# Performance work log

Hardware: AMD Instinct MI355X
Metric: run time of the kernel (lower is better)

Reference implementation:

```python
import jax, jax.numpy as jnp
import numpy as np

DIM = 1  # module init arg; scale = 1/dim**(-0.5) = sqrt(dim)


def setup_inputs() -> dict:
    key = jax.random.key(0)
    kq, kk, kv, km = jax.random.split(key, 4)
    B, Sq, Sk, D = 8, 2048, 2048, 128
    q = jax.random.normal(kq, (B, Sq, D), dtype=jnp.float32)
    k = jax.random.normal(kk, (B, Sk, D), dtype=jnp.float32)
    v = jax.random.normal(kv, (B, Sk, D), dtype=jnp.float32)
    mask = jax.random.uniform(km, (B, Sq, Sk), dtype=jnp.float32)
    return {"q": q, "k": k, "v": v, "mask": mask}


def reference(q, k, v, mask):
    # q = q / dim**(-0.5)  ==  q * sqrt(dim)
    q = q * (DIM ** 0.5)
    # [B, Sq, Sk] scores, multiplicative mask BEFORE softmax
    scores = jnp.einsum("bqd,bkd->bqk", q, k) * mask
    attn = jax.nn.softmax(scores, axis=-1)
    return jnp.einsum("bqk,bkd->bqd", attn, v)
```

## Files before the change

kernel.cpp:

```cpp
#include <hip/hip_runtime.h>
#include <math.h>


typedef short bf16x8 __attribute__((ext_vector_type(8)));
typedef short short4v __attribute__((ext_vector_type(4)));
typedef float f32x4 __attribute__((ext_vector_type(4)));
typedef unsigned short u16x4 __attribute__((ext_vector_type(4)));

#define MFMA16 __builtin_amdgcn_mfma_f32_16x16x32_bf16

namespace {
constexpr int SKn = 2048, DH = 128;
constexpr int QB = 64;
constexpr int NSTEP = 32;

__device__ __forceinline__ unsigned short f2bf(float f) {
    union { float f; unsigned u; } x; x.f = f;
    unsigned r = x.u + 0x7FFFu + ((x.u >> 16) & 1u);
    return (unsigned short)(r >> 16);
}
__device__ __forceinline__ float bf2f(unsigned short h) {
    union { unsigned u; float f; } x; x.u = ((unsigned)h) << 16;
    return x.f;
}
}

__global__ __launch_bounds__(512, 2) void fattn_kernel(
    const float* __restrict__ Q, const float* __restrict__ K,
    const float* __restrict__ V, const float* __restrict__ M,
    float* __restrict__ O)
{
    __shared__ __align__(16) char smem[131072];
    const int bid = blockIdx.x;
    const int b  = bid & 7;
    const int qt = bid >> 3;
    const int tid = threadIdx.x;
    const int lane = tid & 63;
    const int w = tid >> 6;
    const int g2 = w >> 2;
    const int wq = w & 3;
    const int gtid = tid & 255;
    const int m16 = lane & 15;
    const int g = lane >> 4;

    char* slotbase = smem + g2 * 65536;

    const float* Qw = Q + ((size_t)(b * 2048 + qt * QB + wq * 16)) * DH;
    const float* Kb = K + (size_t)b * SKn * DH;
    const float* Vb = V + (size_t)b * SKn * DH;
    const float* Mw = M + ((size_t)(b * 2048 + qt * QB + wq * 16)) * SKn;
    float* Ow = O + ((size_t)(b * 2048 + qt * QB + wq * 16)) * DH;

    bf16x8 qh[4], ql[4];
#pragma unroll
    for (int c = 0; c < 4; ++c) {
        const float* qp = Qw + m16 * DH + c * 32 + g * 8;
        f32x4 a0 = *(const f32x4*)qp;
        f32x4 a1 = *(const f32x4*)(qp + 4);
#pragma unroll
        for (int j = 0; j < 8; ++j) {
            float x = (j < 4) ? a0[j] : a1[j - 4];
            unsigned short h = f2bf(x);
            qh[c][j] = (short)h;
            ql[c][j] = (short)f2bf(x - bf2f(h));
        }
    }

    f32x4 kreg[4], vreg[4];
    f32x4 mreg[2], mreg2[2];
    const int krow = gtid >> 5, kc4 = gtid & 31;
    const int vkv = gtid & 31,  vc8 = gtid >> 5;

    auto kv_of = [&](int t) { return (2 * t + g2) * 32; };

    auto stage_load = [&](int t) {
        const int kv0 = kv_of(t);
#pragma unroll
        for (int i = 0; i < 4; ++i)
            kreg[i] = *(const f32x4*)(Kb + (size_t)(kv0 + i * 8 + krow) * DH + kc4 * 4);
#pragma unroll
        for (int i = 0; i < 4; ++i)
            vreg[i] = *(const f32x4*)(Vb + (size_t)(kv0 + vkv) * DH + (vc8 + i * 8) * 4);
    };

    auto stage_write = [&](int bufsel) {
        char* Khi = slotbase + bufsel * 32768;
        char* Klo = Khi + 8192;
        char* Vhi = Khi + 16384;
        char* Vlo = Khi + 24576;
#pragma unroll
        for (int i = 0; i < 4; ++i) {
            const int row = i * 8 + krow;
            u16x4 h4, l4;
#pragma unroll
            for (int j = 0; j < 4; ++j) {
                unsigned short h = f2bf(kreg[i][j]);
                h4[j] = h;
                l4[j] = f2bf(kreg[i][j] - bf2f(h));
            }
            const int off = row * 256 + ((kc4 * 8) ^ ((row & 15) << 4));
            *(u16x4*)(Khi + off) = h4;
            *(u16x4*)(Klo + off) = l4;
        }
#pragma unroll
        for (int i = 0; i < 4; ++i) {
#pragma unroll
            for (int j = 0; j < 4; ++j) {
                const int d = (vc8 + i * 8) * 4 + j;
                const int off = d * 64 + ((vkv * 2) ^ ((d & 7) << 3));
                unsigned short h = f2bf(vreg[i][j]);
                *(unsigned short*)(Vhi + off) = h;
                *(unsigned short*)(Vlo + off) = f2bf(vreg[i][j] - bf2f(h));
            }
        }
    };

    auto mload = [&](int t, f32x4* dst) {
        const int kv0 = kv_of(t);
#pragma unroll
        for (int nt = 0; nt < 2; ++nt)
            dst[nt] = *(const f32x4*)(Mw + (size_t)m16 * SKn + kv0 + nt * 16 + 4 * g);
    };

    f32x4 o_[8];
#pragma unroll
    for (int nt = 0; nt < 8; ++nt) o_[nt] = 0.f;
    float mrow = -INFINITY, lrow = 0.f;

    stage_load(0);
    mload(0, mreg);
    stage_write(0);
    __syncthreads();

    for (int t = 0; t < NSTEP; ++t) {
        const int cur = t & 1;
        const bool more = (t + 1 < NSTEP);
        if (more) stage_load(t + 1);

        const char* Khi = slotbase + cur * 32768;
        const char* Klo = Khi + 8192;
        f32x4 sT[2];
        sT[0] = 0.f; sT[1] = 0.f;
#pragma unroll
        for (int c = 0; c < 4; ++c) {
#pragma unroll
            for (int nt = 0; nt < 2; ++nt) {
                const int row = nt * 16 + m16;
                const int off = row * 256 + ((c * 64 + g * 16) ^ ((row & 15) << 4));
                bf16x8 ah = *(const bf16x8*)(Khi + off);
                bf16x8 al = *(const bf16x8*)(Klo + off);
                sT[nt] = MFMA16(ah, qh[c], sT[nt], 0, 0, 0);
                sT[nt] = MFMA16(ah, ql[c], sT[nt], 0, 0, 0);
                sT[nt] = MFMA16(al, qh[c], sT[nt], 0, 0, 0);
            }
        }

        if (more) mload(t + 1, mreg2);

        float p[2][4];
        float mx = -INFINITY;
#pragma unroll
        for (int nt = 0; nt < 2; ++nt)
#pragma unroll
            for (int r = 0; r < 4; ++r) {
                p[nt][r] = sT[nt][r] * mreg[nt][r];
                mx = fmaxf(mx, p[nt][r]);
            }
        mx = fmaxf(mx, __shfl_xor(mx, 16));
        mx = fmaxf(mx, __shfl_xor(mx, 32));
        const float mn = fmaxf(mrow, mx);
        const float corr = __expf(mrow - mn);
        mrow = mn;
        float ps = 0.f;
#pragma unroll
        for (int nt = 0; nt < 2; ++nt)
#pragma unroll
            for (int r = 0; r < 4; ++r) {
                p[nt][r] = __expf(p[nt][r] - mn);
                ps += p[nt][r];
            }
        ps += __shfl_xor(ps, 16);
        ps += __shfl_xor(ps, 32);
        lrow = lrow * corr + ps;

        f32x4 corrO;
#pragma unroll
        for (int r = 0; r < 4; ++r) corrO[r] = __shfl(corr, 4 * g + r);
#pragma unroll
        for (int nt = 0; nt < 8; ++nt)
#pragma unroll
            for (int r = 0; r < 4; ++r) o_[nt][r] *= corrO[r];

        bf16x8 ph, pl;
#pragma unroll
        for (int e = 0; e < 8; ++e) {
            const float x = p[e >> 2][e & 3];
            unsigned short h = f2bf(x);
            ph[e] = (short)h;
            pl[e] = (short)f2bf(x - bf2f(h));
        }

        const char* Vhi = Khi + 16384;
        const char* Vlo = Khi + 24576;
#pragma unroll
        for (int nt = 0; nt < 8; ++nt) {
            const int d = nt * 16 + m16;
            const int sw = (d & 7) << 3;
            const int off1 = d * 64 + ((g * 8) ^ sw);
            const int off2 = d * 64 + ((32 + g * 8) ^ sw);
            short4v h1 = *(const short4v*)(Vhi + off1);
            short4v h2 = *(const short4v*)(Vhi + off2);
            short4v l1 = *(const short4v*)(Vlo + off1);
            short4v l2 = *(const short4v*)(Vlo + off2);
            bf16x8 vh = __builtin_shufflevector(h1, h2, 0, 1, 2, 3, 4, 5, 6, 7);
            bf16x8 vl = __builtin_shufflevector(l1, l2, 0, 1, 2, 3, 4, 5, 6, 7);
            o_[nt] = MFMA16(ph, vh, o_[nt], 0, 0, 0);
            o_[nt] = MFMA16(ph, vl, o_[nt], 0, 0, 0);
            o_[nt] = MFMA16(pl, vh, o_[nt], 0, 0, 0);
        }

        if (more) stage_write(cur ^ 1);
        __syncthreads();
        if (more) { mreg[0] = mreg2[0]; mreg[1] = mreg2[1]; }
    }

    if (g2 == 1) {
        char* ob = smem + wq * 8448;
#pragma unroll
        for (int nt = 0; nt < 8; ++nt)
#pragma unroll
            for (int r = 0; r < 4; ++r)
                *(float*)(ob + (4 * g + r) * 528 + (nt * 16 + m16) * 4) = o_[nt][r];
        if (g == 0)
            *(float2*)(smem + 33792 + wq * 128 + m16 * 8) = make_float2(mrow, lrow);
    }
    __syncthreads();
    if (g2 == 0) {
        const float2 ml1 = *(const float2*)(smem + 33792 + wq * 128 + m16 * 8);
        const float ms = fmaxf(mrow, ml1.x);
        const float e0 = __expf(mrow - ms);
        const float e1 = __expf(ml1.x - ms);
        const float inv = 1.f / (lrow * e0 + ml1.y * e1);
        const float a0 = e0 * inv, a1 = e1 * inv;
        f32x4 a0r, a1r;
#pragma unroll
        for (int r = 0; r < 4; ++r) {
            a0r[r] = __shfl(a0, 4 * g + r);
            a1r[r] = __shfl(a1, 4 * g + r);
        }
        const char* ob = smem + wq * 8448;
#pragma unroll
        for (int nt = 0; nt < 8; ++nt)
#pragma unroll
            for (int r = 0; r < 4; ++r) {
                const int d = nt * 16 + m16;
                const float o1 = *(const float*)(ob + (4 * g + r) * 528 + d * 4);
                Ow[(size_t)(4 * g + r) * DH + d] = o_[nt][r] * a0r[r] + o1 * a1r[r];
            }
    }
}

extern "C" void kernel_launch(void* const* d_in, const int* in_sizes, int n_in,
                              void* d_out, int out_size, void* d_ws, size_t ws_size,
                              hipStream_t stream) {
    (void)in_sizes; (void)n_in; (void)out_size; (void)d_ws; (void)ws_size;
    const float* q = (const float*)d_in[0];
    const float* k = (const float*)d_in[1];
    const float* v = (const float*)d_in[2];
    const float* m = (const float*)d_in[3];
    float* o = (float*)d_out;
    fattn_kernel<<<dim3(256), dim3(512), 0, stream>>>(q, k, v, m, o);
}
```

Baseline: 274.3 us.

## Split KV range across two blocks with merge kernel, single-buffer LDS

Splits the key/value sequence into two halves processed by separate blocks, doubling the grid to 512 blocks, and writes partial outputs plus max/sum stats to workspace. A new merge kernel combines the two halves. LDS is halved to a single buffer (double buffering removed, two barriers per step) so more blocks fit per CU, and the bf16 hi/lo split now uses truncation via perm instead of round-to-nearest. The mask is prefetched two steps ahead and MFMA sections get raised priority. The cost is extra workspace traffic, a second launch, and less load/compute overlap.

```diff
diff --git a/kernel.cpp b/kernel.cpp
--- a/kernel.cpp
+++ b/kernel.cpp
@@ -5,14 +5,16 @@
 typedef short bf16x8 __attribute__((ext_vector_type(8)));
 typedef short short4v __attribute__((ext_vector_type(4)));
 typedef float f32x4 __attribute__((ext_vector_type(4)));
-typedef unsigned short u16x4 __attribute__((ext_vector_type(4)));
 
 #define MFMA16 __builtin_amdgcn_mfma_f32_16x16x32_bf16
 
 namespace {
 constexpr int SKn = 2048, DH = 128;
 constexpr int QB = 64;
-constexpr int NSTEP = 32;
+constexpr int ROWS = 8 * 2048;
+constexpr size_t OPART_BYTES = 2ull * ROWS * DH * 4;
+constexpr size_t ML_BYTES = 2ull * ROWS * 8;
+constexpr size_t WS_NEED = OPART_BYTES + ML_BYTES;
 
 __device__ __forceinline__ unsigned short f2bf(float f) {
     union { float f; unsigned u; } x; x.f = f;
@@ -25,15 +27,18 @@
 }
 }
 
-__global__ __launch_bounds__(512, 2) void fattn_kernel(
+__global__ __launch_bounds__(512, 4) void fattn_kernel(
     const float* __restrict__ Q, const float* __restrict__ K,
     const float* __restrict__ V, const float* __restrict__ M,
-    float* __restrict__ O)
+    float* __restrict__ Oout, float2* __restrict__ MLout, const int nkvh)
 {
-    __shared__ __align__(16) char smem[131072];
+    __shared__ __align__(16) char smem[65536];
     const int bid = blockIdx.x;
     const int b  = bid & 7;
-    const int qt = bid >> 3;
+    const int rest = bid >> 3;
+    const int kvh = rest % nkvh;
+    const int qt = rest / nkvh;
+    const int nstep = 16 * (2 / nkvh) * 2 / 2;
     const int tid = threadIdx.x;
     const int lane = tid & 63;
     const int w = tid >> 6;
@@ -43,13 +48,14 @@
     const int m16 = lane & 15;
     const int g = lane >> 4;
 
-    char* slotbase = smem + g2 * 65536;
-
-    const float* Qw = Q + ((size_t)(b * 2048 + qt * QB + wq * 16)) * DH;
+    char* slotbase = smem + g2 * 32768;
+
+    const int rowglobal = b * 2048 + qt * QB + wq * 16;
+    const float* Qw = Q + (size_t)rowglobal * DH;
     const float* Kb = K + (size_t)b * SKn * DH;
     const float* Vb = V + (size_t)b * SKn * DH;
-    const float* Mw = M + ((size_t)(b * 2048 + qt * QB + wq * 16)) * SKn;
-    float* Ow = O + ((size_t)(b * 2048 + qt * QB + wq * 16)) * DH;
+    const float* Mrow = M + (size_t)rowglobal * SKn + (size_t)m16 * SKn;
+    float* Orow = Oout + ((size_t)kvh * ROWS + rowglobal) * DH;
 
     bf16x8 qh[4], ql[4];
 #pragma unroll
@@ -67,11 +73,10 @@
     }
 
     f32x4 kreg[4], vreg[4];
-    f32x4 mreg[2], mreg2[2];
     const int krow = gtid >> 5, kc4 = gtid & 31;
     const int vkv = gtid & 31,  vc8 = gtid >> 5;
 
-    auto kv_of = [&](int t) { return (2 * t + g2) * 32; };
+    auto kv_of = [&](int t) { return kvh * 1024 + (2 * t + g2) * 32; };
 
     auto stage_load = [&](int t) {
         const int kv0 = kv_of(t);
@@ -83,24 +88,29 @@
             vreg[i] = *(const f32x4*)(Vb + (size_t)(kv0 + vkv) * DH + (vc8 + i * 8) * 4);
     };
 
-    auto stage_write = [&](int bufsel) {
-        char* Khi = slotbase + bufsel * 32768;
-        char* Klo = Khi + 8192;
-        char* Vhi = Khi + 16384;
-        char* Vlo = Khi + 24576;
+    auto stage_write = [&]() {
+        char* Khi = slotbase;
+        char* Klo = slotbase + 8192;
+        char* Vhi = slotbase + 16384;
+        char* Vlo = slotbase + 24576;
 #pragma unroll
         for (int i = 0; i < 4; ++i) {
             const int row = i * 8 + krow;
-            u16x4 h4, l4;
-#pragma unroll
-            for (int j = 0; j < 4; ++j) {
-                unsigned short h = f2bf(kreg[i][j]);
-                h4[j] = h;
-                l4[j] = f2bf(kreg[i][j] - bf2f(h));
-            }
+            const unsigned b0 = __float_as_uint(kreg[i][0]);
+            const unsigned b1 = __float_as_uint(kreg[i][1]);
+            const unsigned b2 = __float_as_uint(kreg[i][2]);
+            const unsigned b3 = __float_as_uint(kreg[i][3]);
+            const float r0 = kreg[i][0] - __uint_as_float(b0 & 0xFFFF0000u);
+            const float r1 = kreg[i][1] - __uint_as_float(b1 & 0xFFFF0000u);
+            const float r2 = kreg[i][2] - __uint_as_float(b2 & 0xFFFF0000u);
+            const float r3 = kreg[i][3] - __uint_as_float(b3 & 0xFFFF0000u);
+            const unsigned h01 = __builtin_amdgcn_perm(b1, b0, 0x07060302u);
+            const unsigned h23 = __builtin_amdgcn_perm(b3, b2, 0x07060302u);
+            const unsigned l01 = __builtin_amdgcn_perm(__float_as_uint(r1), __float_as_uint(r0), 0x07060302u);
+            const unsigned l23 = __builtin_amdgcn_perm(__float_as_uint(r3), __float_as_uint(r2), 0x07060302u);
             const int off = row * 256 + ((kc4 * 8) ^ ((row & 15) << 4));
-            *(u16x4*)(Khi + off) = h4;
-            *(u16x4*)(Klo + off) = l4;
+            *(uint2*)(Khi + off) = make_uint2(h01, h23);
+            *(uint2*)(Klo + off) = make_uint2(l01, l23);
         }
 #pragma unroll
         for (int i = 0; i < 4; ++i) {
@@ -108,39 +118,41 @@
             for (int j = 0; j < 4; ++j) {
                 const int d = (vc8 + i * 8) * 4 + j;
                 const int off = d * 64 + ((vkv * 2) ^ ((d & 7) << 3));
-                unsigned short h = f2bf(vreg[i][j]);
-                *(unsigned short*)(Vhi + off) = h;
-                *(unsigned short*)(Vlo + off) = f2bf(vreg[i][j] - bf2f(h));
+                const unsigned bb = __float_as_uint(vreg[i][j]);
+                *(unsigned short*)(Vhi + off) = (unsigned short)(bb >> 16);
+                const float r = vreg[i][j] - __uint_as_float(bb & 0xFFFF0000u);
+                *(unsigned short*)(Vlo + off) = (unsigned short)(__float_as_uint(r) >> 16);
             }
         }
     };
 
-    auto mload = [&](int t, f32x4* dst) {
+    auto mload = [&](int t, f32x4& d0, f32x4& d1) {
         const int kv0 = kv_of(t);
-#pragma unroll
-        for (int nt = 0; nt < 2; ++nt)
-            dst[nt] = *(const f32x4*)(Mw + (size_t)m16 * SKn + kv0 + nt * 16 + 4 * g);
+        d0 = *(const f32x4*)(Mrow + kv0 + 4 * g);
+        d1 = *(const f32x4*)(Mrow + kv0 + 16 + 4 * g);
     };
 
     f32x4 o_[8];
 #pragma unroll
     for (int nt = 0; nt < 8; ++nt) o_[nt] = 0.f;
     float mrow = -INFINITY, lrow = 0.f;
+    f32x4 mA0, mA1, mB0, mB1;
 
     stage_load(0);
-    mload(0, mreg);
-    stage_write(0);
+    mload(0, mA0, mA1);
+    mload(1, mB0, mB1);
+    stage_write();
     __syncthreads();
 
-    for (int t = 0; t < NSTEP; ++t) {
-        const int cur = t & 1;
-        const bool more = (t + 1 < NSTEP);
+    auto step = [&](int t, f32x4& m0, f32x4& m1) {
+        const bool more = (t + 1 < nstep);
         if (more) stage_load(t + 1);
 
-        const char* Khi = slotbase + cur * 32768;
-        const char* Klo = Khi + 8192;
+        const char* Khi = slotbase;
+        const char* Klo = slotbase + 8192;
         f32x4 sT[2];
         sT[0] = 0.f; sT[1] = 0.f;
+        __builtin_amdgcn_s_setprio(1);
 #pragma unroll
         for (int c = 0; c < 4; ++c) {
 #pragma unroll
@@ -154,18 +166,17 @@
                 sT[nt] = MFMA16(al, qh[c], sT[nt], 0, 0, 0);
             }
         }
-
-        if (more) mload(t + 1, mreg2);
+        __builtin_amdgcn_s_setprio(0);
 
         float p[2][4];
         float mx = -INFINITY;
 #pragma unroll
-        for (int nt = 0; nt < 2; ++nt)
-#pragma unroll
-            for (int r = 0; r < 4; ++r) {
-                p[nt][r] = sT[nt][r] * mreg[nt][r];
-                mx = fmaxf(mx, p[nt][r]);
-            }
+        for (int r = 0; r < 4; ++r) {
+            p[0][r] = sT[0][r] * m0[r];
+            p[1][r] = sT[1][r] * m1[r];
+            mx = fmaxf(mx, fmaxf(p[0][r], p[1][r]));
+        }
+        if (t + 2 < nstep) mload(t + 2, m0, m1);
         mx = fmaxf(mx, __shfl_xor(mx, 16));
         mx = fmaxf(mx, __shfl_xor(mx, 32));
         const float mn = fmaxf(mrow, mx);
@@ -191,17 +202,22 @@
 #pragma unroll
             for (int r = 0; r < 4; ++r) o_[nt][r] *= corrO[r];
 
-        bf16x8 ph, pl;
-#pragma unroll
-        for (int e = 0; e < 8; ++e) {
-            const float x = p[e >> 2][e & 3];
-            unsigned short h = f2bf(x);
-            ph[e] = (short)h;
-            pl[e] = (short)f2bf(x - bf2f(h));
-        }
-
-        const char* Vhi = Khi + 16384;
-        const char* Vlo = Khi + 24576;
+        union { unsigned u[4]; bf16x8 v; } PH, PL;
+#pragma unroll
+        for (int e = 0; e < 8; e += 2) {
+            const float x0 = p[e >> 2][e & 3];
+            const float x1 = p[(e + 1) >> 2][(e + 1) & 3];
+            const unsigned c0 = __float_as_uint(x0), c1 = __float_as_uint(x1);
+            PH.u[e >> 1] = __builtin_amdgcn_perm(c1, c0, 0x07060302u);
+            const float r0 = x0 - __uint_as_float(c0 & 0xFFFF0000u);
+            const float r1 = x1 - __uint_as_float(c1 & 0xFFFF0000u);
+            PL.u[e >> 1] = __builtin_amdgcn_perm(__float_as_uint(r1), __float_as_uint(r0), 0x07060302u);
+        }
+        const bf16x8 ph = PH.v, pl = PL.v;
+
+        const char* Vhi = slotbase + 16384;
+        const char* Vlo = slotbase + 24576;
+        __builtin_amdgcn_s_setprio(1);
 #pragma unroll
         for (int nt = 0; nt < 8; ++nt) {
             const int d = nt * 16 + m16;
@@ -218,10 +234,16 @@
             o_[nt] = MFMA16(ph, vl, o_[nt], 0, 0, 0);
             o_[nt] = MFMA16(pl, vh, o_[nt], 0, 0, 0);
         }
-
-        if (more) stage_write(cur ^ 1);
+        __builtin_amdgcn_s_setprio(0);
+
         __syncthreads();
-        if (more) { mreg[0] = mreg2[0]; mreg[1] = mreg2[1]; }
+        if (more) stage_write();
+        __syncthreads();
+    };
+
+    for (int t = 0; t < nstep; t += 2) {
+        step(t, mA0, mA1);
+        step(t + 1, mB0, mB1);
     }
 
     if (g2 == 1) {
@@ -240,8 +262,11 @@
         const float ms = fmaxf(mrow, ml1.x);
         const float e0 = __expf(mrow - ms);
         const float e1 = __expf(ml1.x - ms);
-        const float inv = 1.f / (lrow * e0 + ml1.y * e1);
+        const float lcomb = lrow * e0 + ml1.y * e1;
+        const float inv = 1.f / lcomb;
         const float a0 = e0 * inv, a1 = e1 * inv;
+        if (nkvh == 2 && g == 0)
+            MLout[(size_t)kvh * ROWS + rowglobal + m16] = make_float2(ms, lcomb);
         f32x4 a0r, a1r;
 #pragma unroll
         for (int r = 0; r < 4; ++r) {
@@ -255,19 +280,48 @@
             for (int r = 0; r < 4; ++r) {
                 const int d = nt * 16 + m16;
                 const float o1 = *(const float*)(ob + (4 * g + r) * 528 + d * 4);
-                Ow[(size_t)(4 * g + r) * DH + d] = o_[nt][r] * a0r[r] + o1 * a1r[r];
+                Orow[(size_t)(4 * g + r) * DH + d] = o_[nt][r] * a0r[r] + o1 * a1r[r];
             }
     }
+}
+
+__global__ __launch_bounds__(256) void merge_kernel(
+    const float* __restrict__ Op, const float2* __restrict__ ml, float* __restrict__ O)
+{
+    const int fi = blockIdx.x * 256 + threadIdx.x;
+    const int row = fi >> 5, c = fi & 31;
+    const float2 a = ml[row];
+    const float2 bml = ml[row + ROWS];
+    const float ms = fmaxf(a.x, bml.x);
+    const float w0 = __expf(a.x - ms) * a.y;
+    const float w1 = __expf(bml.x - ms) * bml.y;
+    const float inv = 1.f / (w0 + w1);
+    const float s0 = w0 * inv, s1 = w1 * inv;
+    const float4 o0 = *(const float4*)(Op + ((size_t)row << 7) + (c << 2));
+    const float4 o1 = *(const float4*)(Op + ((size_t)(row + ROWS) << 7) + (c << 2));
+    float4 o;
+    o.x = s0 * o0.x + s1 * o1.x;
+    o.y = s0 * o0.y + s1 * o1.y;
+    o.z = s0 * o0.z + s1 * o1.z;
+    o.w = s0 * o0.w + s1 * o1.w;
+    *(float4*)(O + ((size_t)row << 7) + (c << 2)) = o;
 }
 
 extern "C" void kernel_launch(void* const* d_in, const int* in_sizes, int n_in,
                               void* d_out, int out_size, void* d_ws, size_t ws_size,
                               hipStream_t stream) {
-    (void)in_sizes; (void)n_in; (void)out_size; (void)d_ws; (void)ws_size;
+    (void)in_sizes; (void)n_in; (void)out_size;
     const float* q = (const float*)d_in[0];
     const float* k = (const float*)d_in[1];
     const float* v = (const float*)d_in[2];
     const float* m = (const float*)d_in[3];
     float* o = (float*)d_out;
-    fattn_kernel<<<dim3(256), dim3(512), 0, stream>>>(q, k, v, m, o);
-}
+    if (ws_size >= WS_NEED) {
+        float* opart = (float*)d_ws;
+        float2* ml = (float2*)((char*)d_ws + OPART_BYTES);
+        fattn_kernel<<<dim3(512), dim3(512), 0, stream>>>(q, k, v, m, opart, ml, 2);
+        merge_kernel<<<dim3(2048), dim3(256), 0, stream>>>(opart, ml, o);
+    } else {
+        fattn_kernel<<<dim3(256), dim3(512), 0, stream>>>(q, k, v, m, o, nullptr, 1);
+    }
+}
```

Result: slower. 470.5 us (+71.5%).
